# Optimization experiments

Hardware: AMD Instinct MI355X
Metric: run time of the kernel (lower is better)

Reference implementation:

```python
import jax, jax.numpy as jnp
import numpy as np

B, D_IN, D_S = 16384, 1024, 1024


def setup_inputs() -> dict:
    key = jax.random.key(0)
    ks = jax.random.split(key, 7)
    s_in = 1.0 / np.sqrt(D_IN)
    s_h = 1.0 / np.sqrt(D_S)
    return {
        "input": jax.random.normal(ks[0], (B, D_IN), jnp.float32),
        "cell_state": jax.random.normal(ks[1], (B, D_S), jnp.float32),
        "hidden_state": jax.random.normal(ks[2], (B, D_S), jnp.float32),
        "Wx": jax.random.uniform(ks[3], (4, D_S, D_IN), jnp.float32, -s_in, s_in),
        "bx": jax.random.uniform(ks[4], (4, D_S), jnp.float32, -s_in, s_in),
        "Wh": jax.random.uniform(ks[5], (4, D_S, D_S), jnp.float32, -s_h, s_h),
        "bh": jax.random.uniform(ks[6], (4, D_S), jnp.float32, -s_h, s_h),
    }


def reference(input, cell_state, hidden_state, Wx, bx, Wh, bh):
    # Fused: two batched GEMMs produce all 4 gate pre-activations.
    # gates_x, gates_h: [4, B, D_S]; gate order: forget, input, cand, output
    gx = jnp.einsum('bi,gsi->gbs', input, Wx) + bx[:, None, :]
    gh = jnp.einsum('bh,gsh->gbs', hidden_state, Wh) + bh[:, None, :]
    pre = gx + gh
    f = jax.nn.sigmoid(pre[0])
    i = jax.nn.sigmoid(pre[1]) * jnp.tanh(pre[2])
    new_cell_state = cell_state * f + i
    output = jnp.tanh(new_cell_state) * jax.nn.sigmoid(pre[3])
    return (new_cell_state, output)
```

## Files before the change

kernel.cpp:

```cpp
#include <hip/hip_runtime.h>
#include <hip/hip_bf16.h>
#include <stdint.h>


typedef short bf16x8 __attribute__((ext_vector_type(8)));
typedef float f32x4 __attribute__((ext_vector_type(4)));

#define B_ROWS 16384
#define D_K 2048

__device__ __forceinline__ unsigned short f2bf(float f) {
    unsigned u = __builtin_bit_cast(unsigned, f);
    u += 0x7FFFu + ((u >> 16) & 1u);
    return (unsigned short)(u >> 16);
}

__device__ __forceinline__ float sigf(float x) { return 1.0f / (1.0f + __expf(-x)); }
__device__ __forceinline__ float tanhfast(float x) { return 2.0f / (1.0f + __expf(-2.0f * x)) - 1.0f; }

#define GLD16(gp, lp)                                                          \
    __builtin_amdgcn_global_load_lds(                                          \
        (const __attribute__((address_space(1))) unsigned int*)(gp),           \
        (__attribute__((address_space(3))) unsigned int*)(lp), 16, 0, 0)

#define FENCE() asm volatile("" ::: "memory")


__global__ void pack_A_kernel(const float* __restrict__ x,
                              const float* __restrict__ h,
                              unsigned short* __restrict__ A) {
    const int total = B_ROWS * (D_K / 4);
    for (int v = blockIdx.x * blockDim.x + threadIdx.x; v < total;
         v += gridDim.x * blockDim.x) {
        const int b = v >> 9;
        const int k0 = (v & 511) << 2;
        const float* src = (k0 < 1024) ? (x + (size_t)b * 1024 + k0)
                                       : (h + (size_t)b * 1024 + (k0 - 1024));
        float4 f = *(const float4*)src;
        unsigned p0 = (unsigned)f2bf(f.x) | ((unsigned)f2bf(f.y) << 16);
        unsigned p1 = (unsigned)f2bf(f.z) | ((unsigned)f2bf(f.w) << 16);
        uint2 o; o.x = p0; o.y = p1;
        *(uint2*)(A + (size_t)v * 4) = o;
    }
}

__global__ void pack_W_kernel(const float* __restrict__ Wx,
                              const float* __restrict__ Wh,
                              unsigned short* __restrict__ W) {
    const int total = 4096 * (D_K / 4);
    for (int v = blockIdx.x * blockDim.x + threadIdx.x; v < total;
         v += gridDim.x * blockDim.x) {
        const int n = v >> 9;
        const int k0 = (v & 511) << 2;
        const float* src = (k0 < 1024) ? (Wx + (size_t)n * 1024 + k0)
                                       : (Wh + (size_t)n * 1024 + (k0 - 1024));
        float4 f = *(const float4*)src;
        unsigned p0 = (unsigned)f2bf(f.x) | ((unsigned)f2bf(f.y) << 16);
        unsigned p1 = (unsigned)f2bf(f.z) | ((unsigned)f2bf(f.w) << 16);
        uint2 o; o.x = p0; o.y = p1;
        *(uint2*)(W + (size_t)v * 4) = o;
    }
}

__global__ void pack_bias_kernel(const float* __restrict__ bx,
                                 const float* __restrict__ bh,
                                 float* __restrict__ bias) {
    int i = blockIdx.x * blockDim.x + threadIdx.x;
    if (i < 4096) bias[i] = bx[i] + bh[i];
}


__global__ __launch_bounds__(512, 4) void lstm_gemm_kernel(
    const unsigned short* __restrict__ A,
    const unsigned short* __restrict__ W,
    const float* __restrict__ bias,
    const float* __restrict__ cell,
    float* __restrict__ out) {
    __shared__ __align__(16) unsigned short smem[2][12288];

    const int bid = blockIdx.x;
    const int wgi = (bid & 7) * 256 + (bid >> 3);
    const int brow = (wgi & 127) << 7;
    const int bcol = (wgi >> 7) << 6;

    const int tid = threadIdx.x;
    const int wid = tid >> 6;
    const int lane = tid & 63;
    const int wr = wid >> 2;
    const int wc = wid & 3;
    const int lr = lane & 15, lg = lane >> 4;
    const int l16 = lane >> 2;
    const int lk = (((lane & 3) ^ ((lane >> 3) & 3)) << 3);

    f32x4 acc[4][4];
#pragma unroll
    for (int g = 0; g < 4; ++g)
#pragma unroll
        for (int m = 0; m < 4; ++m) acc[g][m] = (f32x4){0.f, 0.f, 0.f, 0.f};

    const unsigned short* gp[3];
#pragma unroll
    for (int i = 0; i < 3; ++i) {
        const int c = wid * 3 + i;
        if (c < 8) {
            gp[i] = A + (size_t)(brow + c * 16 + l16) * D_K + lk;
        } else {
            const int cw = c - 8;
            gp[i] = W + (size_t)((cw >> 2) * 1024 + bcol + (cw & 3) * 16 + l16) * D_K + lk;
        }
    }

#define STAGE(buf, kt)                                                         \
    do {                                                                       \
        char* _d = (char*)smem[buf] + (wid * 3) * 1024;                        \
        _Pragma("unroll")                                                      \
        for (int _i = 0; _i < 3; ++_i) GLD16(gp[_i] + (kt), _d + _i * 1024);   \
    } while (0)

#define COMPUTE(buf)                                                           \
    do {                                                                       \
        const unsigned short* _sb = smem[buf];                                 \
        const int _sl = ((lg ^ ((lr >> 1) & 3)) << 3);                         \
        bf16x8 a[4], w[4];                                                     \
        _Pragma("unroll")                                                      \
        for (int m = 0; m < 4; ++m)                                            \
            a[m] = *(const bf16x8*)&_sb[(wr * 4 + m) * 512 + lr * 32 + _sl];   \
        _Pragma("unroll")                                                      \
        for (int g = 0; g < 4; ++g)                                            \
            w[g] = *(const bf16x8*)&_sb[(8 + g * 4 + wc) * 512 + lr * 32 + _sl]; \
        __builtin_amdgcn_s_setprio(1);                                         \
        _Pragma("unroll")                                                      \
        for (int g = 0; g < 4; ++g) {                                          \
            _Pragma("unroll")                                                  \
            for (int m = 0; m < 4; ++m)                                        \
                acc[g][m] = __builtin_amdgcn_mfma_f32_16x16x32_bf16(           \
                    a[m], w[g], acc[g][m], 0, 0, 0);                           \
        }                                                                      \
        __builtin_amdgcn_s_setprio(0);                                         \
    } while (0)

    STAGE(0, 0);

    for (int t = 0; t < 63; ++t) {
        STAGE((t + 1) & 1, (t + 1) * 32);
        asm volatile("s_waitcnt vmcnt(3)" ::: "memory");
        __builtin_amdgcn_s_barrier();
        FENCE();
        COMPUTE(t & 1);
        FENCE();
        __builtin_amdgcn_s_barrier();
        FENCE();
    }
    asm volatile("s_waitcnt vmcnt(0)" ::: "memory");
    __builtin_amdgcn_s_barrier();
    FENCE();
    COMPUTE(1);

#undef STAGE
#undef COMPUTE

    float bv[4];
#pragma unroll
    for (int g = 0; g < 4; ++g) bv[g] = bias[(g << 10) + bcol + wc * 16 + lr];

    float* outc = out;
    float* outh = out + (size_t)B_ROWS * 1024;
#pragma unroll
    for (int m = 0; m < 4; ++m) {
#pragma unroll
        for (int r = 0; r < 4; ++r) {
            const int b = brow + wr * 64 + m * 16 + lg * 4 + r;
            const size_t idx = (size_t)b * 1024 + bcol + wc * 16 + lr;
            float pf = acc[0][m][r] + bv[0];
            float pi = acc[1][m][r] + bv[1];
            float pc = acc[2][m][r] + bv[2];
            float po = acc[3][m][r] + bv[3];
            float cl = cell[idx];
            float nc = cl * sigf(pf) + sigf(pi) * tanhfast(pc);
            outc[idx] = nc;
            outh[idx] = tanhfast(nc) * sigf(po);
        }
    }
}


__global__ void lstm_naive_kernel(const float* __restrict__ x,
                                  const float* __restrict__ cell,
                                  const float* __restrict__ h,
                                  const float* __restrict__ Wx,
                                  const float* __restrict__ bx,
                                  const float* __restrict__ Wh,
                                  const float* __restrict__ bh,
                                  float* __restrict__ out) {
    int idx = blockIdx.x * blockDim.x + threadIdx.x;
    if (idx >= B_ROWS * 1024) return;
    int b = idx >> 10, s = idx & 1023;
    const float* xr = x + (size_t)b * 1024;
    const float* hr = h + (size_t)b * 1024;
    float pre[4];
#pragma unroll
    for (int g = 0; g < 4; ++g) {
        float acc = bx[(g << 10) + s] + bh[(g << 10) + s];
        const float* wx = Wx + ((size_t)(g << 10) + s) * 1024;
        const float* wh = Wh + ((size_t)(g << 10) + s) * 1024;
        for (int k = 0; k < 1024; ++k) acc += xr[k] * wx[k] + hr[k] * wh[k];
        pre[g] = acc;
    }
    float nc = cell[idx] * sigf(pre[0]) + sigf(pre[1]) * tanhfast(pre[2]);
    out[idx] = nc;
    out[(size_t)B_ROWS * 1024 + idx] = tanhfast(nc) * sigf(pre[3]);
}


extern "C" void kernel_launch(void* const* d_in, const int* in_sizes, int n_in,
                              void* d_out, int out_size, void* d_ws, size_t ws_size,
                              hipStream_t stream) {
    const float* x    = (const float*)d_in[0];
    const float* cell = (const float*)d_in[1];
    const float* hid  = (const float*)d_in[2];
    const float* Wx   = (const float*)d_in[3];
    const float* bx   = (const float*)d_in[4];
    const float* Wh   = (const float*)d_in[5];
    const float* bh   = (const float*)d_in[6];
    float* out = (float*)d_out;

    const size_t szA = (size_t)B_ROWS * D_K * 2;
    const size_t szW = (size_t)4096 * D_K * 2;
    const size_t szB = 4096 * 4;
    if (ws_size < szA + szW + szB) {
        lstm_naive_kernel<<<(B_ROWS * 1024) / 256, 256, 0, stream>>>(
            x, cell, hid, Wx, bx, Wh, bh, out);
        return;
    }

    unsigned short* Ab = (unsigned short*)d_ws;
    unsigned short* Wb = (unsigned short*)((char*)d_ws + szA);
    float* bias = (float*)((char*)d_ws + szA + szW);

    pack_A_kernel<<<8192, 256, 0, stream>>>(x, hid, Ab);
    pack_W_kernel<<<2048, 256, 0, stream>>>(Wx, Wh, Wb);
    pack_bias_kernel<<<16, 256, 0, stream>>>(bx, bh, bias);

    lstm_gemm_kernel<<<2048, 512, 0, stream>>>(Ab, Wb, bias, cell, out);
}
```

Before: 369.1 us.

## Use 64-wide K tiles with double-buffered A and single-buffered W

```diff
diff --git a/kernel.cpp b/kernel.cpp
--- a/kernel.cpp
+++ b/kernel.cpp
@@ -70,18 +70,19 @@
 }
 
 
-__global__ __launch_bounds__(512, 4) void lstm_gemm_kernel(
+__global__ __launch_bounds__(512, 2) void lstm_gemm_kernel(
     const unsigned short* __restrict__ A,
     const unsigned short* __restrict__ W,
     const float* __restrict__ bias,
     const float* __restrict__ cell,
     float* __restrict__ out) {
-    __shared__ __align__(16) unsigned short smem[2][12288];
+    __shared__ __align__(16) unsigned short sA[2][8192];
+    __shared__ __align__(16) unsigned short sW[16384];
 
     const int bid = blockIdx.x;
-    const int wgi = (bid & 7) * 256 + (bid >> 3);
-    const int brow = (wgi & 127) << 7;
-    const int bcol = (wgi >> 7) << 6;
+    const int wg = (bid & 7) * 256 + (bid >> 3);
+    const int brow = (wg >> 4) << 7;
+    const int bcol = (wg & 15) << 6;
 
     const int tid = threadIdx.x;
     const int wid = tid >> 6;
@@ -89,8 +90,8 @@
     const int wr = wid >> 2;
     const int wc = wid & 3;
     const int lr = lane & 15, lg = lane >> 4;
-    const int l16 = lane >> 2;
-    const int lk = (((lane & 3) ^ ((lane >> 3) & 3)) << 3);
+    const int l8 = lane >> 3;
+    const int lcol = (((lane & 7) ^ l8) << 3);
 
     f32x4 acc[4][4];
 #pragma unroll
@@ -98,65 +99,78 @@
 #pragma unroll
         for (int m = 0; m < 4; ++m) acc[g][m] = (f32x4){0.f, 0.f, 0.f, 0.f};
 
-    const unsigned short* gp[3];
-#pragma unroll
-    for (int i = 0; i < 3; ++i) {
-        const int c = wid * 3 + i;
-        if (c < 8) {
-            gp[i] = A + (size_t)(brow + c * 16 + l16) * D_K + lk;
-        } else {
-            const int cw = c - 8;
-            gp[i] = W + (size_t)((cw >> 2) * 1024 + bcol + (cw & 3) * 16 + l16) * D_K + lk;
-        }
-    }
-
-#define STAGE(buf, kt)                                                         \
+    const unsigned short* gpA[2];
+#pragma unroll
+    for (int i = 0; i < 2; ++i) {
+        const int c = wid * 2 + i;
+        gpA[i] = A + (size_t)(brow + c * 8 + l8) * D_K + lcol;
+    }
+    const unsigned short* gpW[4];
+#pragma unroll
+    for (int i = 0; i < 4; ++i) {
+        const int cw = wid * 4 + i;
+        gpW[i] = W + (size_t)((cw >> 3) * 1024 + bcol + (cw & 7) * 8 + l8) * D_K + lcol;
+    }
+
+#define STAGE_A(buf, kt)                                                       \
     do {                                                                       \
-        char* _d = (char*)smem[buf] + (wid * 3) * 1024;                        \
+        GLD16(gpA[0] + (kt), (char*)sA[buf] + (wid * 2) * 1024);               \
+        GLD16(gpA[1] + (kt), (char*)sA[buf] + (wid * 2 + 1) * 1024);           \
+    } while (0)
+
+#define STAGE_W(kt)                                                            \
+    do {                                                                       \
         _Pragma("unroll")                                                      \
-        for (int _i = 0; _i < 3; ++_i) GLD16(gp[_i] + (kt), _d + _i * 1024);   \
+        for (int _i = 0; _i < 4; ++_i)                                         \
+            GLD16(gpW[_i] + (kt), (char*)sW + (wid * 4 + _i) * 1024);          \
     } while (0)
 
 #define COMPUTE(buf)                                                           \
     do {                                                                       \
-        const unsigned short* _sb = smem[buf];                                 \
-        const int _sl = ((lg ^ ((lr >> 1) & 3)) << 3);                         \
-        bf16x8 a[4], w[4];                                                     \
+        const unsigned short* _sa = sA[buf];                                   \
         _Pragma("unroll")                                                      \
-        for (int m = 0; m < 4; ++m)                                            \
-            a[m] = *(const bf16x8*)&_sb[(wr * 4 + m) * 512 + lr * 32 + _sl];   \
-        _Pragma("unroll")                                                      \
-        for (int g = 0; g < 4; ++g)                                            \
-            w[g] = *(const bf16x8*)&_sb[(8 + g * 4 + wc) * 512 + lr * 32 + _sl]; \
-        __builtin_amdgcn_s_setprio(1);                                         \
-        _Pragma("unroll")                                                      \
-        for (int g = 0; g < 4; ++g) {                                          \
+        for (int kk = 0; kk < 2; ++kk) {                                       \
+            const int swk = (kk * 32 + lg * 8) ^ ((lr & 7) << 3);              \
+            bf16x8 a[4], w[4];                                                 \
             _Pragma("unroll")                                                  \
             for (int m = 0; m < 4; ++m)                                        \
-                acc[g][m] = __builtin_amdgcn_mfma_f32_16x16x32_bf16(           \
-                    a[m], w[g], acc[g][m], 0, 0, 0);                           \
+                a[m] = *(const bf16x8*)&_sa[(wr * 64 + m * 16 + lr) * 64 + swk]; \
+            _Pragma("unroll")                                                  \
+            for (int g = 0; g < 4; ++g)                                        \
+                w[g] = *(const bf16x8*)&sW[(g * 64 + wc * 16 + lr) * 64 + swk]; \
+            __builtin_amdgcn_s_setprio(1);                                     \
+            _Pragma("unroll")                                                  \
+            for (int g = 0; g < 4; ++g) {                                      \
+                _Pragma("unroll")                                              \
+                for (int m = 0; m < 4; ++m)                                    \
+                    acc[g][m] = __builtin_amdgcn_mfma_f32_16x16x32_bf16(       \
+                        a[m], w[g], acc[g][m], 0, 0, 0);                       \
+            }                                                                  \
+            __builtin_amdgcn_s_setprio(0);                                     \
         }                                                                      \
-        __builtin_amdgcn_s_setprio(0);                                         \
     } while (0)
 
-    STAGE(0, 0);
-
-    for (int t = 0; t < 63; ++t) {
-        STAGE((t + 1) & 1, (t + 1) * 32);
-        asm volatile("s_waitcnt vmcnt(3)" ::: "memory");
+    STAGE_A(0, 0);
+    STAGE_W(0);
+
+    for (int t = 0; t < 31; ++t) {
+        STAGE_A((t + 1) & 1, (t + 1) * 64);
+        asm volatile("s_waitcnt vmcnt(2)" ::: "memory");
         __builtin_amdgcn_s_barrier();
         FENCE();
         COMPUTE(t & 1);
         FENCE();
         __builtin_amdgcn_s_barrier();
         FENCE();
+        STAGE_W((t + 1) * 64);
     }
     asm volatile("s_waitcnt vmcnt(0)" ::: "memory");
     __builtin_amdgcn_s_barrier();
     FENCE();
     COMPUTE(1);
 
-#undef STAGE
+#undef STAGE_A
+#undef STAGE_W
 #undef COMPUTE
 
     float bv[4];
```

Result: slower. 426.6 us (+15.6%).
